# Optimization experiments

Measured on AMD Instinct MI355X. Metric: run time of the kernel, lower is better.

## Reference

```python
import math
import jax, jax.numpy as jnp
import numpy as np


def setup_inputs() -> dict:
    key = jax.random.key(0)
    k1, k2 = jax.random.split(key)
    B, Sq, Sk, H, D = 2, 2048, 2048, 16, 128
    q = jax.random.normal(k1, (B, Sq, H, D), dtype=jnp.float32)
    kv = jax.random.normal(k2, (B, Sk, 2, H, D), dtype=jnp.float32)
    return {"q": q, "kv": kv}


def reference(q, kv):
    # CrossAttention.forward with causal=True, softmax_scale=None,
    # attention_dropout=0.0, key_padding_mask=None.
    B, Sq, H, D = q.shape
    Sk = kv.shape[1]
    k = kv[:, :, 0]  # (B, Sk, H, D)
    v = kv[:, :, 1]  # (B, Sk, H, D)
    softmax_scale = 1.0 / math.sqrt(D)
    # scores: (B, H, Sq, Sk)
    scores = jnp.einsum("bthd,bshd->bhts", q, k * softmax_scale)
    # causal mask: col_idx > row_idx + Sk - Sq  -> masked with -10000 (not -inf),
    # exactly as the torch code does.
    row_idx = jnp.arange(Sq, dtype=jnp.int32)[:, None]
    col_idx = jnp.arange(Sk, dtype=jnp.int32)[None, :]
    causal_mask = col_idx > row_idx + (Sk - Sq)  # (Sq, Sk)
    scores = jnp.where(causal_mask[None, None, :, :], jnp.float32(-10000.0), scores)
    attention = jax.nn.softmax(scores, axis=-1)
    # output: (B, Sq, H, D)
    output = jnp.einsum("bhts,bshd->bthd", attention, v)
    return output
```

## Files before the change

### kernel.cpp

```cpp
#include <hip/hip_runtime.h>
#include <stdint.h>
#include <math.h>

typedef __attribute__((ext_vector_type(8))) __bf16 bf16x8;
typedef __attribute__((ext_vector_type(4))) __bf16 bf16x4;
typedef __attribute__((ext_vector_type(4))) float f32x4;
typedef __attribute__((ext_vector_type(16))) float f32x16;
typedef __attribute__((ext_vector_type(4))) uint32_t u32x4;

constexpr int B = 2, SQ = 2048, SK = 2048, H = 16, D = 128;
constexpr int KVB = 64;
constexpr int NT = SK / KVB;
constexpr int RS = 2 * H * D;
constexpr size_t TILE_B = (size_t)KVB * D * 2;
constexpr size_t KWS_B = (size_t)B * H * NT * TILE_B;
constexpr float SCL2E = 0.08838834764831845f * 1.4426950408889634f;

#define AS1 __attribute__((address_space(1)))
#define AS3 __attribute__((address_space(3)))
__device__ __forceinline__ void gl_lds16(const char* g, char* l) {
  __builtin_amdgcn_global_load_lds((const AS1 char*)g, (AS3 char*)l, 16, 0, 0);
}

__global__ __launch_bounds__(256) void conv_kv(
    const float* __restrict__ kv, char* __restrict__ kws, char* __restrict__ vws)
{
  __shared__ __bf16 Vst[64 * 136];
  const int bid = blockIdx.x;
  const int bh = bid >> 5, t = bid & 31;
  const int b = bh >> 4, h = bh & 15;
  const float* Kg = kv + (size_t)b * SK * RS + (size_t)h * D + (size_t)t * KVB * RS;
  const float* Vg = Kg + H * D;
  char* kt = kws + (size_t)bid * TILE_B;
  char* vt = vws + (size_t)bid * TILE_B;
  const int tid = threadIdx.x;

  #pragma unroll
  for (int it = 0; it < 4; ++it) {
    int c = tid + it * 256;
    int s = c >> 4, dc = c & 15;
    {
      f32x4 a = *(const f32x4*)(Kg + (size_t)s * RS + dc * 8);
      f32x4 bb = *(const f32x4*)(Kg + (size_t)s * RS + dc * 8 + 4);
      bf16x8 w;
      #pragma unroll
      for (int j = 0; j < 4; ++j) { w[j] = (__bf16)a[j]; w[4 + j] = (__bf16)bb[j]; }
      *(bf16x8*)(kt + s * 256 + ((dc * 16) ^ ((s & 7) << 4))) = w;
    }
    {
      f32x4 a = *(const f32x4*)(Vg + (size_t)s * RS + dc * 8);
      f32x4 bb = *(const f32x4*)(Vg + (size_t)s * RS + dc * 8 + 4);
      bf16x4 w0, w1;
      #pragma unroll
      for (int j = 0; j < 4; ++j) { w0[j] = (__bf16)a[j]; w1[j] = (__bf16)bb[j]; }
      *(bf16x4*)&Vst[s * 136 + dc * 8] = w0;
      *(bf16x4*)&Vst[s * 136 + dc * 8 + 4] = w1;
    }
  }
  __syncthreads();
  #pragma unroll
  for (int it = 0; it < 4; ++it) {
    int c = tid + it * 256;
    int d = c >> 3, sc = c & 7;
    bf16x8 w;
    #pragma unroll
    for (int j = 0; j < 8; ++j) w[j] = Vst[(sc * 8 + j) * 136 + d];
    *(bf16x8*)(vt + d * 128 + ((sc * 16) ^ ((d & 7) << 4))) = w;
  }
}

__global__ __launch_bounds__(256, 2) void fa_fwd(
    const float* __restrict__ q, const char* __restrict__ kws,
    const char* __restrict__ vws, float* __restrict__ out)
{
  __shared__ __align__(16) char Klds[2][16384];
  __shared__ __align__(16) char Vlds[2][16384];
  __shared__ float Lsh[4][32];

  const int tid  = threadIdx.x;
  const int wave = tid >> 6;
  const int lane = tid & 63;
  const int l32  = lane & 31;
  const int hb   = lane >> 5;
  const int xk   = (l32 & 7) << 4;

  const int bid = blockIdx.x;
  const int bh  = bid & 31;
  const int qt  = 15 - (bid >> 5);
  const int b   = bh >> 4, h = bh & 15;
  const int q0w = qt * 128 + wave * 32;
  const int nT  = 2 * qt + 2;
  const int t_d = (q0w + 31) >> 6;

  const char* ktb = kws + (size_t)bh * NT * TILE_B;
  const char* vtb = vws + (size_t)bh * NT * TILE_B;

  auto STAGE = [&](int buf, int t) {
    const char* kt = ktb + (size_t)t * TILE_B + wave * 4096 + lane * 16;
    const char* vt = vtb + (size_t)t * TILE_B + wave * 4096 + lane * 16;
    char* kl = &Klds[buf][wave * 4096];
    char* vl = &Vlds[buf][wave * 4096];
    #pragma unroll
    for (int i = 0; i < 4; ++i) gl_lds16(kt + i * 1024, kl + i * 1024);
    #pragma unroll
    for (int i = 0; i < 4; ++i) gl_lds16(vt + i * 1024, vl + i * 1024);
  };

  STAGE(0, 0);

  const float* Qg = q + (((size_t)b * SQ + q0w + l32) * H + h) * D;
  bf16x8 qf[8];
  #pragma unroll
  for (int ks = 0; ks < 8; ++ks) {
    f32x4 a = *(const f32x4*)(Qg + ks * 16 + hb * 8);
    f32x4 c = *(const f32x4*)(Qg + ks * 16 + hb * 8 + 4);
    #pragma unroll
    for (int j = 0; j < 4; ++j) {
      qf[ks][j]     = (__bf16)(a[j] * SCL2E);
      qf[ks][4 + j] = (__bf16)(c[j] * SCL2E);
    }
  }

  f32x16 o[4];
  #pragma unroll
  for (int nd = 0; nd < 4; ++nd)
    #pragma unroll
    for (int r = 0; r < 16; ++r) o[nd][r] = 0.f;
  float l_run = 0.f;

  int cur = 0;
  for (int t = 0; t < nT; ++t) {
    __syncthreads();
    if (t + 1 < nT) STAGE(cur ^ 1, t + 1);

    if (t <= t_d) {
      const char* kb = Klds[cur];
      const char* vbB = Vlds[cur];

      f32x16 s0, s1;
      #pragma unroll
      for (int r = 0; r < 16; ++r) { s0[r] = 0.f; s1[r] = 0.f; }
      #pragma unroll
      for (int ks = 0; ks < 8; ++ks) {
        bf16x8 k0 = *(const bf16x8*)(kb + l32 * 256 + (((ks * 2 + hb) * 16) ^ xk));
        bf16x8 k1 = *(const bf16x8*)(kb + (32 + l32) * 256 + (((ks * 2 + hb) * 16) ^ xk));
        s0 = __builtin_amdgcn_mfma_f32_32x32x16_bf16(k0, qf[ks], s0, 0, 0, 0);
        s1 = __builtin_amdgcn_mfma_f32_32x32x16_bf16(k1, qf[ks], s1, 0, 0, 0);
      }

      float p[32];
      #pragma unroll
      for (int r = 0; r < 16; ++r) {
        p[r]      = exp2f(s0[r]);
        p[16 + r] = exp2f(s1[r]);
      }
      if (t == t_d) {
        const int qg = q0w + l32;
        #pragma unroll
        for (int r = 0; r < 32; ++r) {
          int kvg = t * 64 + (r & 3) + 8 * ((r >> 2) & 3) + 4 * hb + 32 * (r >> 4);
          if (kvg > qg) p[r] = 0.f;
        }
      }
      float a0 = 0.f, a1 = 0.f, a2 = 0.f, a3 = 0.f;
      #pragma unroll
      for (int r = 0; r < 32; r += 4) {
        a0 += p[r]; a1 += p[r + 1]; a2 += p[r + 2]; a3 += p[r + 3];
      }
      l_run += (a0 + a1) + (a2 + a3);

      bf16x8 pa[4];
      #pragma unroll
      for (int ks = 0; ks < 4; ++ks) {
        const int bs = ks * 8;
        uint32_t w0, w1, w2, w3;
        asm("v_cvt_pk_bf16_f32 %0, %1, %2" : "=v"(w0) : "v"(p[bs + 0]), "v"(p[bs + 1]));
        asm("v_cvt_pk_bf16_f32 %0, %1, %2" : "=v"(w1) : "v"(p[bs + 2]), "v"(p[bs + 3]));
        asm("v_cvt_pk_bf16_f32 %0, %1, %2" : "=v"(w2) : "v"(p[bs + 4]), "v"(p[bs + 5]));
        asm("v_cvt_pk_bf16_f32 %0, %1, %2" : "=v"(w3) : "v"(p[bs + 6]), "v"(p[bs + 7]));
        asm("v_permlane32_swap_b32 %0, %1" : "+v"(w0), "+v"(w2));
        asm("v_permlane32_swap_b32 %0, %1" : "+v"(w1), "+v"(w3));
        u32x4 uw; uw[0] = w0; uw[1] = w1; uw[2] = w2; uw[3] = w3;
        pa[ks] = __builtin_bit_cast(bf16x8, uw);
      }

      #pragma unroll
      for (int nd = 0; nd < 4; ++nd) {
        #pragma unroll
        for (int ks = 0; ks < 4; ++ks) {
          bf16x8 vb = *(const bf16x8*)(vbB + (nd * 32 + l32) * 128 + (((ks * 2 + hb) * 16) ^ xk));
          o[nd] = __builtin_amdgcn_mfma_f32_32x32x16_bf16(pa[ks], vb, o[nd], 0, 0, 0);
        }
      }
    }
    cur ^= 1;
  }

  float la = l_run, lb = l_run;
  asm("v_permlane32_swap_b32 %0, %1" : "+v"(la), "+v"(lb));
  float l_tot = la + lb;
  if (hb == 0) Lsh[wave][l32] = l_tot;
  __syncthreads();

  float invl[16];
  #pragma unroll
  for (int r = 0; r < 16; ++r)
    invl[r] = 1.0f / Lsh[wave][(r & 3) + 8 * (r >> 2) + 4 * hb];

  #pragma unroll
  for (int r = 0; r < 16; ++r) {
    const int qrow = q0w + (r & 3) + 8 * (r >> 2) + 4 * hb;
    float* Og = out + (((size_t)b * SQ + qrow) * H + h) * D + l32;
    #pragma unroll
    for (int nd = 0; nd < 4; ++nd)
      Og[nd * 32] = o[nd][r] * invl[r];
  }
}

extern "C" void kernel_launch(void* const* d_in, const int* in_sizes, int n_in,
                              void* d_out, int out_size, void* d_ws, size_t ws_size,
                              hipStream_t stream) {
  const float* q  = (const float*)d_in[0];
  const float* kv = (const float*)d_in[1];
  float* out = (float*)d_out;
  char* kws = (char*)d_ws;
  char* vws = kws + KWS_B;
  conv_kv<<<dim3(B * H * NT), dim3(256), 0, stream>>>(kv, kws, vws);
  fa_fwd<<<dim3(16 * 32), dim3(256), 0, stream>>>(q, kws, vws, out);
}
```

Baseline: 85.25 us.

## Pre-swizzle K/V into MFMA fragment order and read directly from global

The conversion kernel now writes K and V tiles in per-lane MFMA fragment order, so the attention kernel loads operands straight from global memory (through L2) with one coalesced 16-byte load per lane. This removes the LDS double buffer and the per-tile block barriers. Each wave is assigned a paired low/high query chunk to balance causal work and iterates only over its own tiles. It also skips the upper half of the diagonal tile and uses raw v_exp_f32. The trade-off is that repeated K/V reads now rely on L2/cache hits instead of LDS sharing across the four waves, and global load latency is no longer hidden by explicit prefetching.

```diff
diff --git a/kernel.cpp b/kernel.cpp
--- a/kernel.cpp
+++ b/kernel.cpp
@@ -1,9 +1,7 @@
 #include <hip/hip_runtime.h>
 #include <stdint.h>
-#include <math.h>
 
 typedef __attribute__((ext_vector_type(8))) __bf16 bf16x8;
-typedef __attribute__((ext_vector_type(4))) __bf16 bf16x4;
 typedef __attribute__((ext_vector_type(4))) float f32x4;
 typedef __attribute__((ext_vector_type(16))) float f32x16;
 typedef __attribute__((ext_vector_type(4))) uint32_t u32x4;
@@ -16,23 +14,24 @@
 constexpr size_t KWS_B = (size_t)B * H * NT * TILE_B;
 constexpr float SCL2E = 0.08838834764831845f * 1.4426950408889634f;
 
-#define AS1 __attribute__((address_space(1)))
-#define AS3 __attribute__((address_space(3)))
-__device__ __forceinline__ void gl_lds16(const char* g, char* l) {
-  __builtin_amdgcn_global_load_lds((const AS1 char*)g, (AS3 char*)l, 16, 0, 0);
+__device__ __forceinline__ float fexp2(float x) {
+  float r;
+  asm("v_exp_f32 %0, %1" : "=v"(r) : "v"(x));
+  return r;
 }
 
 __global__ __launch_bounds__(256) void conv_kv(
-    const float* __restrict__ kv, char* __restrict__ kws, char* __restrict__ vws)
+    const float* __restrict__ kv, char* __restrict__ kfr, char* __restrict__ vfr)
 {
+  __shared__ __bf16 Kst[64 * 136];
   __shared__ __bf16 Vst[64 * 136];
   const int bid = blockIdx.x;
   const int bh = bid >> 5, t = bid & 31;
   const int b = bh >> 4, h = bh & 15;
   const float* Kg = kv + (size_t)b * SK * RS + (size_t)h * D + (size_t)t * KVB * RS;
   const float* Vg = Kg + H * D;
-  char* kt = kws + (size_t)bid * TILE_B;
-  char* vt = vws + (size_t)bid * TILE_B;
+  char* kt = kfr + (size_t)bid * TILE_B;
+  char* vt = vfr + (size_t)bid * TILE_B;
   const int tid = threadIdx.x;
 
   #pragma unroll
@@ -45,36 +44,44 @@
       bf16x8 w;
       #pragma unroll
       for (int j = 0; j < 4; ++j) { w[j] = (__bf16)a[j]; w[4 + j] = (__bf16)bb[j]; }
-      *(bf16x8*)(kt + s * 256 + ((dc * 16) ^ ((s & 7) << 4))) = w;
+      *(bf16x8*)&Kst[s * 136 + dc * 8] = w;
     }
     {
       f32x4 a = *(const f32x4*)(Vg + (size_t)s * RS + dc * 8);
       f32x4 bb = *(const f32x4*)(Vg + (size_t)s * RS + dc * 8 + 4);
-      bf16x4 w0, w1;
-      #pragma unroll
-      for (int j = 0; j < 4; ++j) { w0[j] = (__bf16)a[j]; w1[j] = (__bf16)bb[j]; }
-      *(bf16x4*)&Vst[s * 136 + dc * 8] = w0;
-      *(bf16x4*)&Vst[s * 136 + dc * 8 + 4] = w1;
+      bf16x8 w;
+      #pragma unroll
+      for (int j = 0; j < 4; ++j) { w[j] = (__bf16)a[j]; w[4 + j] = (__bf16)bb[j]; }
+      *(bf16x8*)&Vst[s * 136 + dc * 8] = w;
     }
   }
   __syncthreads();
   #pragma unroll
   for (int it = 0; it < 4; ++it) {
     int c = tid + it * 256;
-    int d = c >> 3, sc = c & 7;
-    bf16x8 w;
-    #pragma unroll
-    for (int j = 0; j < 8; ++j) w[j] = Vst[(sc * 8 + j) * 136 + d];
-    *(bf16x8*)(vt + d * 128 + ((sc * 16) ^ ((d & 7) << 4))) = w;
+    {
+      int ks = c >> 7, rg = (c >> 6) & 1, ln = c & 63;
+      int row = rg * 32 + (ln & 31);
+      int d0 = ks * 16 + (ln >> 5) * 8;
+      bf16x8 w = *(const bf16x8*)&Kst[row * 136 + d0];
+      *(bf16x8*)(kt + c * 16) = w;
+    }
+    {
+      int nd = c >> 8, k2 = (c >> 6) & 3, ln = c & 63;
+      int d = nd * 32 + (ln & 31);
+      int sv = k2 * 16 + (ln >> 5) * 8;
+      bf16x8 w;
+      #pragma unroll
+      for (int j = 0; j < 8; ++j) w[j] = Vst[(sv + j) * 136 + d];
+      *(bf16x8*)(vt + c * 16) = w;
+    }
   }
 }
 
 __global__ __launch_bounds__(256, 2) void fa_fwd(
-    const float* __restrict__ q, const char* __restrict__ kws,
-    const char* __restrict__ vws, float* __restrict__ out)
+    const float* __restrict__ q, const char* __restrict__ kfr,
+    const char* __restrict__ vfr, float* __restrict__ out)
 {
-  __shared__ __align__(16) char Klds[2][16384];
-  __shared__ __align__(16) char Vlds[2][16384];
   __shared__ float Lsh[4][32];
 
   const int tid  = threadIdx.x;
@@ -82,31 +89,18 @@
   const int lane = tid & 63;
   const int l32  = lane & 31;
   const int hb   = lane >> 5;
-  const int xk   = (l32 & 7) << 4;
 
   const int bid = blockIdx.x;
   const int bh  = bid & 31;
-  const int qt  = 15 - (bid >> 5);
+  const int g   = bid >> 5;
   const int b   = bh >> 4, h = bh & 15;
-  const int q0w = qt * 128 + wave * 32;
-  const int nT  = 2 * qt + 2;
-  const int t_d = (q0w + 31) >> 6;
-
-  const char* ktb = kws + (size_t)bh * NT * TILE_B;
-  const char* vtb = vws + (size_t)bh * NT * TILE_B;
-
-  auto STAGE = [&](int buf, int t) {
-    const char* kt = ktb + (size_t)t * TILE_B + wave * 4096 + lane * 16;
-    const char* vt = vtb + (size_t)t * TILE_B + wave * 4096 + lane * 16;
-    char* kl = &Klds[buf][wave * 4096];
-    char* vl = &Vlds[buf][wave * 4096];
-    #pragma unroll
-    for (int i = 0; i < 4; ++i) gl_lds16(kt + i * 1024, kl + i * 1024);
-    #pragma unroll
-    for (int i = 0; i < 4; ++i) gl_lds16(vt + i * 1024, vl + i * 1024);
-  };
-
-  STAGE(0, 0);
+  const int qu  = (wave < 2) ? (2 * g + wave) : (62 - 2 * g + (wave - 2));
+  const int q0w = qu * 32;
+  const int t_d = qu >> 1;
+  const int nTw = t_d + 1;
+
+  const char* kt0 = kfr + (size_t)bh * NT * TILE_B;
+  const char* vt0 = vfr + (size_t)bh * NT * TILE_B;
 
   const float* Qg = q + (((size_t)b * SQ + q0w + l32) * H + h) * D;
   bf16x8 qf[8];
@@ -128,72 +122,83 @@
     for (int r = 0; r < 16; ++r) o[nd][r] = 0.f;
   float l_run = 0.f;
 
-  int cur = 0;
-  for (int t = 0; t < nT; ++t) {
-    __syncthreads();
-    if (t + 1 < nT) STAGE(cur ^ 1, t + 1);
-
-    if (t <= t_d) {
-      const char* kb = Klds[cur];
-      const char* vbB = Vlds[cur];
-
-      f32x16 s0, s1;
-      #pragma unroll
-      for (int r = 0; r < 16; ++r) { s0[r] = 0.f; s1[r] = 0.f; }
+  for (int t = 0; t < nTw; ++t) {
+    const char* kb = kt0 + (size_t)t * TILE_B;
+    const char* vb0 = vt0 + (size_t)t * TILE_B;
+    const bool khi = (t < t_d) || (qu & 1);
+
+    f32x16 s0, s1;
+    #pragma unroll
+    for (int r = 0; r < 16; ++r) { s0[r] = 0.f; s1[r] = 0.f; }
+    #pragma unroll
+    for (int ks = 0; ks < 8; ++ks) {
+      bf16x8 k0 = *(const bf16x8*)(kb + (size_t)(ks * 2) * 1024 + lane * 16);
+      s0 = __builtin_amdgcn_mfma_f32_32x32x16_bf16(k0, qf[ks], s0, 0, 0, 0);
+    }
+    if (khi) {
       #pragma unroll
       for (int ks = 0; ks < 8; ++ks) {
-        bf16x8 k0 = *(const bf16x8*)(kb + l32 * 256 + (((ks * 2 + hb) * 16) ^ xk));
-        bf16x8 k1 = *(const bf16x8*)(kb + (32 + l32) * 256 + (((ks * 2 + hb) * 16) ^ xk));
-        s0 = __builtin_amdgcn_mfma_f32_32x32x16_bf16(k0, qf[ks], s0, 0, 0, 0);
+        bf16x8 k1 = *(const bf16x8*)(kb + (size_t)(ks * 2 + 1) * 1024 + lane * 16);
         s1 = __builtin_amdgcn_mfma_f32_32x32x16_bf16(k1, qf[ks], s1, 0, 0, 0);
       }
-
-      float p[32];
-      #pragma unroll
-      for (int r = 0; r < 16; ++r) {
-        p[r]      = exp2f(s0[r]);
-        p[16 + r] = exp2f(s1[r]);
-      }
-      if (t == t_d) {
-        const int qg = q0w + l32;
+    }
+
+    float p[32];
+    #pragma unroll
+    for (int r = 0; r < 16; ++r) p[r] = fexp2(s0[r]);
+    if (khi) {
+      #pragma unroll
+      for (int r = 0; r < 16; ++r) p[16 + r] = fexp2(s1[r]);
+    }
+    if (t == t_d) {
+      const int qg = q0w + l32;
+      #pragma unroll
+      for (int r = 0; r < 32; ++r) {
+        if (r >= 16 && !khi) continue;
+        int kvg = t * 64 + (r & 3) + 8 * ((r >> 2) & 3) + 4 * hb + 32 * (r >> 4);
+        if (kvg > qg) p[r] = 0.f;
+      }
+    }
+    {
+      float a0 = 0.f, a1 = 0.f, a2 = 0.f, a3 = 0.f;
+      #pragma unroll
+      for (int r = 0; r < 16; r += 4) {
+        a0 += p[r]; a1 += p[r + 1]; a2 += p[r + 2]; a3 += p[r + 3];
+      }
+      if (khi) {
         #pragma unroll
-        for (int r = 0; r < 32; ++r) {
-          int kvg = t * 64 + (r & 3) + 8 * ((r >> 2) & 3) + 4 * hb + 32 * (r >> 4);
-          if (kvg > qg) p[r] = 0.f;
+        for (int r = 16; r < 32; r += 4) {
+          a0 += p[r]; a1 += p[r + 1]; a2 += p[r + 2]; a3 += p[r + 3];
         }
       }
-      float a0 = 0.f, a1 = 0.f, a2 = 0.f, a3 = 0.f;
-      #pragma unroll
-      for (int r = 0; r < 32; r += 4) {
-        a0 += p[r]; a1 += p[r + 1]; a2 += p[r + 2]; a3 += p[r + 3];
-      }
       l_run += (a0 + a1) + (a2 + a3);
-
-      bf16x8 pa[4];
+    }
+
+    bf16x8 pa[4];
+    #pragma unroll
+    for (int ks = 0; ks < 4; ++ks) {
+      if (ks >= 2 && !khi) continue;
+      const int bs = ks * 8;
+      uint32_t w0, w1, w2, w3;
+      asm("v_cvt_pk_bf16_f32 %0, %1, %2" : "=v"(w0) : "v"(p[bs + 0]), "v"(p[bs + 1]));
+      asm("v_cvt_pk_bf16_f32 %0, %1, %2" : "=v"(w1) : "v"(p[bs + 2]), "v"(p[bs + 3]));
+      asm("v_cvt_pk_bf16_f32 %0, %1, %2" : "=v"(w2) : "v"(p[bs + 4]), "v"(p[bs + 5]));
+      asm("v_cvt_pk_bf16_f32 %0, %1, %2" : "=v"(w3) : "v"(p[bs + 6]), "v"(p[bs + 7]));
+      asm("v_permlane32_swap_b32 %0, %1" : "+v"(w0), "+v"(w2));
+      asm("v_permlane32_swap_b32 %0, %1" : "+v"(w1), "+v"(w3));
+      u32x4 uw; uw[0] = w0; uw[1] = w1; uw[2] = w2; uw[3] = w3;
+      pa[ks] = __builtin_bit_cast(bf16x8, uw);
+    }
+
+    #pragma unroll
+    for (int nd = 0; nd < 4; ++nd) {
       #pragma unroll
       for (int ks = 0; ks < 4; ++ks) {
-        const int bs = ks * 8;
-        uint32_t w0, w1, w2, w3;
-        asm("v_cvt_pk_bf16_f32 %0, %1, %2" : "=v"(w0) : "v"(p[bs + 0]), "v"(p[bs + 1]));
-        asm("v_cvt_pk_bf16_f32 %0, %1, %2" : "=v"(w1) : "v"(p[bs + 2]), "v"(p[bs + 3]));
-        asm("v_cvt_pk_bf16_f32 %0, %1, %2" : "=v"(w2) : "v"(p[bs + 4]), "v"(p[bs + 5]));
-        asm("v_cvt_pk_bf16_f32 %0, %1, %2" : "=v"(w3) : "v"(p[bs + 6]), "v"(p[bs + 7]));
-        asm("v_permlane32_swap_b32 %0, %1" : "+v"(w0), "+v"(w2));
-        asm("v_permlane32_swap_b32 %0, %1" : "+v"(w1), "+v"(w3));
-        u32x4 uw; uw[0] = w0; uw[1] = w1; uw[2] = w2; uw[3] = w3;
-        pa[ks] = __builtin_bit_cast(bf16x8, uw);
-      }
-
-      #pragma unroll
-      for (int nd = 0; nd < 4; ++nd) {
-        #pragma unroll
-        for (int ks = 0; ks < 4; ++ks) {
-          bf16x8 vb = *(const bf16x8*)(vbB + (nd * 32 + l32) * 128 + (((ks * 2 + hb) * 16) ^ xk));
-          o[nd] = __builtin_amdgcn_mfma_f32_32x32x16_bf16(pa[ks], vb, o[nd], 0, 0, 0);
-        }
-      }
-    }
-    cur ^= 1;
+        if (ks >= 2 && !khi) continue;
+        bf16x8 vb = *(const bf16x8*)(vb0 + (size_t)(nd * 4 + ks) * 1024 + lane * 16);
+        o[nd] = __builtin_amdgcn_mfma_f32_32x32x16_bf16(pa[ks], vb, o[nd], 0, 0, 0);
+      }
+    }
   }
 
   float la = l_run, lb = l_run;
@@ -223,8 +228,8 @@
   const float* q  = (const float*)d_in[0];
   const float* kv = (const float*)d_in[1];
   float* out = (float*)d_out;
-  char* kws = (char*)d_ws;
-  char* vws = kws + KWS_B;
-  conv_kv<<<dim3(B * H * NT), dim3(256), 0, stream>>>(kv, kws, vws);
-  fa_fwd<<<dim3(16 * 32), dim3(256), 0, stream>>>(q, kws, vws, out);
-}
+  char* kfr = (char*)d_ws;
+  char* vfr = kfr + KWS_B;
+  conv_kv<<<dim3(B * H * NT), dim3(256), 0, stream>>>(kv, kfr, vfr);
+  fa_fwd<<<dim3(16 * 32), dim3(256), 0, stream>>>(q, kfr, vfr, out);
+}
```

Result: slower. 167.1 us (+96.0%).
